# Kernel tuning notes

Measured on AMD Instinct MI355X. Metric: run time of the kernel, lower is better.

## Reference

```python
import jax, jax.numpy as jnp
import numpy as np

EMBED_DIM = 1024
NUM_HEADS = 16
HEAD_DIM = EMBED_DIM // NUM_HEADS
EPS = 1e-6
B, T = 4, 8192


def setup_inputs() -> dict:
    key = jax.random.key(0)
    ks = jax.random.split(key, 11)
    s = 1.0 / np.sqrt(EMBED_DIM)
    inp = {
        'query': jax.random.normal(ks[0], (B, T, EMBED_DIM), jnp.float32),
        'key': jax.random.normal(ks[1], (B, T, EMBED_DIM), jnp.float32),
        'value': jax.random.normal(ks[2], (B, T, EMBED_DIM), jnp.float32),
        'Wq': jax.random.normal(ks[3], (EMBED_DIM, EMBED_DIM), jnp.float32) * s,
        'bq': jnp.zeros((EMBED_DIM,), jnp.float32),
        'Wk': jax.random.normal(ks[4], (EMBED_DIM, EMBED_DIM), jnp.float32) * s,
        'bk': jnp.zeros((EMBED_DIM,), jnp.float32),
        'Wv': jax.random.normal(ks[5], (EMBED_DIM, EMBED_DIM), jnp.float32) * s,
        'bv': jnp.zeros((EMBED_DIM,), jnp.float32),
        'Wo': jax.random.normal(ks[6], (EMBED_DIM, EMBED_DIM), jnp.float32) * s,
        'bo': jnp.zeros((EMBED_DIM,), jnp.float32),
    }
    return inp


def _feature_map(x):
    return jax.nn.elu(x) + 1.0


def reference(query, key, value, Wq, bq, Wk, bk, Wv, bv, Wo, bo):
    b, t, _ = query.shape
    # projections (torch Linear: x @ W.T + b)
    q = query @ Wq.T + bq
    k = key @ Wk.T + bk
    v = value @ Wv.T + bv
    # split heads -> (b, h, t, d)
    def split(x):
        return x.reshape(b, t, NUM_HEADS, HEAD_DIM).transpose(0, 2, 1, 3)
    q = _feature_map(split(q))
    k = _feature_map(split(k))
    v = split(v)
    k_sum = k.sum(axis=2)                                   # (b,h,d)
    denom = jnp.einsum('bhtd,bhd->bht', q, k_sum) + EPS     # (b,h,t)
    kv = jnp.einsum('bhtd,bhtv->bhdv', k, v)                # (b,h,d,d)
    out = jnp.einsum('bhtd,bhde->bhte', q, kv) / denom[..., None]
    out = out.transpose(0, 2, 1, 3).reshape(b, t, EMBED_DIM)
    return out @ Wo.T + bo
```

## Files before the change

### kernel.cpp

```cpp
#include <hip/hip_runtime.h>
#include <hip/hip_bf16.h>

typedef long long TLONG;
typedef float  f32x4_t  __attribute__((ext_vector_type(4)));
typedef short  s16x8_t  __attribute__((ext_vector_type(8)));
typedef short  s16x4_t  __attribute__((ext_vector_type(4)));
typedef __bf16 bf16x8_t __attribute__((ext_vector_type(8)));

#define MDIM 32768
#define NDIM 1024
#define KDIM 1024
#define EPSV 1e-6f

#define BARRIER() asm volatile("s_barrier" ::: "memory")
#define SBAR() __builtin_amdgcn_sched_barrier(0)

__device__ __forceinline__ unsigned short f2bf_bits(float f) {
  __hip_bfloat16 h = __float2bfloat16(f);
  return __builtin_bit_cast(unsigned short, h);
}
__device__ __forceinline__ float bf2f(unsigned short u) {
  unsigned int x = ((unsigned int)u) << 16;
  return __builtin_bit_cast(float, x);
}
__device__ __forceinline__ void load_lds16(const void* g, void* l) {
  __builtin_amdgcn_global_load_lds((const __attribute__((address_space(1))) void*)g,
                                   (__attribute__((address_space(3))) void*)l, 16, 0, 0);
}

__device__ __forceinline__ void conv8(const float* __restrict__ in,
                                      unsigned short* __restrict__ out, TLONG i) {
  f32x4_t a = __builtin_nontemporal_load(reinterpret_cast<const f32x4_t*>(in + i));
  f32x4_t b = __builtin_nontemporal_load(reinterpret_cast<const f32x4_t*>(in + i + 4));
  s16x8_t o;
  o[0] = (short)f2bf_bits(a[0]); o[1] = (short)f2bf_bits(a[1]);
  o[2] = (short)f2bf_bits(a[2]); o[3] = (short)f2bf_bits(a[3]);
  o[4] = (short)f2bf_bits(b[0]); o[5] = (short)f2bf_bits(b[1]);
  o[6] = (short)f2bf_bits(b[2]); o[7] = (short)f2bf_bits(b[3]);
  *reinterpret_cast<s16x8_t*>(out + i) = o;
}

__global__ __launch_bounds__(256) void convert_all_f32_bf16(
    const float* __restrict__ q, const float* __restrict__ k, const float* __restrict__ v,
    const float* __restrict__ wq, const float* __restrict__ wk,
    const float* __restrict__ wv, const float* __restrict__ wo,
    unsigned short* __restrict__ oq, unsigned short* __restrict__ ok,
    unsigned short* __restrict__ ov, unsigned short* __restrict__ owq,
    unsigned short* __restrict__ owk, unsigned short* __restrict__ owv,
    unsigned short* __restrict__ owo) {
  int blk = blockIdx.x;
  if (blk < 6144) {
    const float* in; unsigned short* out;
    if (blk < 2048)      { in = q; out = oq; }
    else if (blk < 4096) { in = k; out = ok; blk -= 2048; }
    else                 { in = v; out = ov; blk -= 4096; }
    const TLONG n = 33554432LL;
    TLONG i = ((TLONG)blk * 256 + threadIdx.x) * 8;
    const TLONG stride = 2048LL * 256 * 8;
    for (; i < n; i += stride) conv8(in, out, i);
  } else {
    blk -= 6144;
    const float* in; unsigned short* out;
    if (blk < 512)       { in = wq; out = owq; }
    else if (blk < 1024) { in = wk; out = owk; blk -= 512; }
    else if (blk < 1536) { in = wv; out = owv; blk -= 1024; }
    else                 { in = wo; out = owo; blk -= 1536; }
    TLONG i = ((TLONG)blk * 256 + threadIdx.x) * 8;
    conv8(in, out, i);
  }
}

template <int FMAP, int OUT>
__global__ __launch_bounds__(512, 2) void gemm256(
    const unsigned short* __restrict__ A, const unsigned short* __restrict__ W,
    const float* __restrict__ bias, void* __restrict__ Cout) {
  __shared__ short lds[65536];
  const int bid = blockIdx.x;
  const int swz = (bid & 7) * 64 + (bid >> 3);
  const int mt = swz >> 2;
  const int nt = swz & 3;

  const int tid = threadIdx.x;
  const int lane = tid & 63;
  const int w = tid >> 6;
  const int wr = w >> 2, wc = w & 3;
  const int l15 = lane & 15, lh = lane >> 4;

  const int arow0 = mt * 256, brow0 = nt * 256;

  auto stage_half = [&](const unsigned short* __restrict__ src, int ldsOff,
                        int grow, int k0) {
#pragma unroll
    for (int i = 0; i < 2; ++i) {
      const int c = i * 512 + tid;
      const int r = c >> 3, ps = c & 7;
      load_lds16(src + (grow + r) * KDIM + k0 + ((ps ^ (r & 7)) * 8),
                 &lds[ldsOff + c * 8]);
    }
  };

  f32x4_t acc[8][4];
#pragma unroll
  for (int m = 0; m < 8; ++m)
#pragma unroll
    for (int n = 0; n < 4; ++n) acc[m][n] = (f32x4_t)0.0f;

  s16x8_t Af[8][2], Bf[4][2];

  auto rdA = [&](int pb, int m, int ks) -> s16x8_t {
    const int row = wr * 128 + m * 16 + l15;
    return *reinterpret_cast<const s16x8_t*>(
        &lds[pb + row * 64 + (((ks * 4 + lh) ^ (row & 7)) * 8)]);
  };
  auto rdB = [&](int pb, int n, int ks) -> s16x8_t {
    const int row = wc * 64 + n * 16 + l15;
    return *reinterpret_cast<const s16x8_t*>(
        &lds[pb + 16384 + row * 64 + (((ks * 4 + lh) ^ (row & 7)) * 8)]);
  };
  auto quad = [&](int mb, int nl) {
    __builtin_amdgcn_s_setprio(1);
#pragma unroll
    for (int m = 0; m < 4; ++m)
#pragma unroll
      for (int n = 0; n < 2; ++n)
#pragma unroll
        for (int ks = 0; ks < 2; ++ks)
          acc[mb + m][nl + n] = __builtin_amdgcn_mfma_f32_16x16x32_bf16(
              __builtin_bit_cast(bf16x8_t, Af[mb + m][ks]),
              __builtin_bit_cast(bf16x8_t, Bf[nl + n][ks]),
              acc[mb + m][nl + n], 0, 0, 0);
    __builtin_amdgcn_s_setprio(0);
  };

  stage_half(A, 0,             arow0,       0);
  stage_half(A, 8192,          arow0 + 128, 0);
  stage_half(W, 16384,         brow0,       0);
  stage_half(W, 16384 + 8192,  brow0 + 128, 0);
  stage_half(A, 32768,         arow0,       64);
  stage_half(A, 32768 + 8192,  arow0 + 128, 64);
  asm volatile("s_waitcnt vmcnt(4)" ::: "memory");
  SBAR();
  BARRIER();

  for (int kt = 0; kt < 16; ++kt) {
    const int p = kt & 1;
    const int pb = p * 32768, qb = 32768 - pb;
    const int k1 = ((kt + 1) & 15) * 64;
    const int k2 = ((kt + 2) & 15) * 64;
#pragma unroll
    for (int m = 0; m < 4; ++m)
#pragma unroll
      for (int ks = 0; ks < 2; ++ks) Af[m][ks] = rdA(pb, m, ks);
#pragma unroll
    for (int n = 0; n < 2; ++n)
#pragma unroll
      for (int ks = 0; ks < 2; ++ks) Bf[n][ks] = rdB(pb, n, ks);
    SBAR();
#pragma unroll
    for (int m = 0; m < 4; ++m)
#pragma unroll
      for (int ks = 0; ks < 2; ++ks) Af[4 + m][ks] = rdA(pb, 4 + m, ks);
    SBAR();
#pragma unroll
    for (int n = 2; n < 4; ++n)
#pragma unroll
      for (int ks = 0; ks < 2; ++ks) Bf[n][ks] = rdB(pb, n, ks);
    SBAR();
    stage_half(W, qb + 16384, brow0, k1);
    BARRIER();
    asm volatile("s_waitcnt lgkmcnt(12)" ::: "memory");
    SBAR();
    quad(0, 0);
    BARRIER();
    stage_half(W, qb + 16384 + 8192, brow0 + 128, k1);
    BARRIER();
    asm volatile("s_waitcnt lgkmcnt(4)" ::: "memory");
    SBAR();
    quad(4, 0);
    BARRIER();
    stage_half(A, pb, arow0, k2);
    BARRIER();
    asm volatile("s_waitcnt lgkmcnt(0)" ::: "memory");
    SBAR();
    quad(0, 2);
    BARRIER();
    stage_half(A, pb + 8192, arow0 + 128, k2);
    BARRIER();
    quad(4, 2);
    asm volatile("s_waitcnt vmcnt(4)" ::: "memory");
    SBAR();
    BARRIER();
  }

  if (OUT == 2) {
    asm volatile("s_waitcnt vmcnt(0)" ::: "memory");
    SBAR();
    BARRIER();
#pragma unroll
    for (int n = 0; n < 4; ++n) {
      const int colL = wc * 64 + n * 16 + l15;
      const float bv = bias[nt * 256 + colL];
      const int xr = (colL & 31) * 8;
#pragma unroll
      for (int m = 0; m < 8; ++m) {
        const int rowL = wr * 128 + m * 16 + lh * 4;
        s16x4_t o;
#pragma unroll
        for (int j = 0; j < 4; ++j) {
          float v = acc[m][n][j] + bv;
          if (FMAP) v = (v > 0.0f) ? (v + 1.0f) : __expf(v);
          o[j] = (short)f2bf_bits(v);
        }
        *reinterpret_cast<s16x4_t*>(&lds[colL * 256 + (rowL ^ xr)]) = o;
      }
    }
    BARRIER();
    const int colL = tid >> 1;
    const int half = tid & 1;
    const int col = nt * 256 + colL;
    const int gh = col >> 6, gd = col & 63;
    const int gb = (mt * 256) >> 13;
    const int tl0 = (mt * 256) & 8191;
    const int xr = (colL & 31) * 8;
    unsigned short* outp = reinterpret_cast<unsigned short*>(Cout) +
        (((TLONG)(gb * 16 + gh) * 64 + gd) * 8192 + tl0 + half * 128);
#pragma unroll
    for (int k = 0; k < 16; ++k) {
      const int row = half * 128 + k * 8;
      s16x8_t v = *reinterpret_cast<const s16x8_t*>(&lds[colL * 256 + (row ^ xr)]);
      *reinterpret_cast<s16x8_t*>(outp + k * 8) = v;
    }
  } else {
#pragma unroll
    for (int n = 0; n < 4; ++n) {
      const int col = nt * 256 + wc * 64 + n * 16 + l15;
      const float bv = bias[col];
#pragma unroll
      for (int m = 0; m < 8; ++m) {
        const int row0 = mt * 256 + wr * 128 + m * 16 + lh * 4;
#pragma unroll
        for (int j = 0; j < 4; ++j) {
          float v = acc[m][n][j] + bv;
          if (FMAP) v = (v > 0.0f) ? (v + 1.0f) : __expf(v);
          if (OUT == 1)
            __builtin_nontemporal_store(v,
                &reinterpret_cast<float*>(Cout)[(row0 + j) * NDIM + col]);
          else
            reinterpret_cast<unsigned short*>(Cout)[(row0 + j) * NDIM + col] = f2bf_bits(v);
        }
      }
    }
  }
}

__global__ __launch_bounds__(256) void kv_ksum_mfma(
    const unsigned short* __restrict__ kT, const unsigned short* __restrict__ vT,
    float* __restrict__ kvT, float* __restrict__ ksum) {
  const int bid = blockIdx.x;
  const int bh = bid >> 4, ch = bid & 15;
  const int tid = threadIdx.x;
  const int lane = tid & 63, w = tid >> 6;
  const int l15 = lane & 15, lh = lane >> 4;
  const int dblk = (w >> 1) * 32, eblk = (w & 1) * 32;

  f32x4_t acc[2][2];
#pragma unroll
  for (int m = 0; m < 2; ++m)
#pragma unroll
    for (int n = 0; n < 2; ++n) acc[m][n] = (f32x4_t)0.0f;
  float ks0 = 0.f, ks1 = 0.f;

  const int tbase = ch * 512 + lh * 8;
  const unsigned short* ka = kT + (bh * 64 + dblk + l15) * 8192 + tbase;
  const unsigned short* va = vT + (bh * 64 + eblk + l15) * 8192 + tbase;

  for (int t0 = 0; t0 < 512; t0 += 32) {
    s16x8_t ar[2], br[2];
#pragma unroll
    for (int m = 0; m < 2; ++m)
      ar[m] = *reinterpret_cast<const s16x8_t*>(ka + m * 16 * 8192 + t0);
#pragma unroll
    for (int n = 0; n < 2; ++n)
      br[n] = *reinterpret_cast<const s16x8_t*>(va + n * 16 * 8192 + t0);
#pragma unroll
    for (int m = 0; m < 2; ++m)
#pragma unroll
      for (int n = 0; n < 2; ++n)
        acc[m][n] = __builtin_amdgcn_mfma_f32_16x16x32_bf16(
            __builtin_bit_cast(bf16x8_t, ar[m]),
            __builtin_bit_cast(bf16x8_t, br[n]), acc[m][n], 0, 0, 0);
    if (eblk == 0) {
#pragma unroll
      for (int i = 0; i < 8; ++i) ks0 += bf2f((unsigned short)ar[0][i]);
#pragma unroll
      for (int i = 0; i < 8; ++i) ks1 += bf2f((unsigned short)ar[1][i]);
    }
  }

  if (eblk == 0) {
    ks0 += __shfl_xor(ks0, 16); ks0 += __shfl_xor(ks0, 32);
    ks1 += __shfl_xor(ks1, 16); ks1 += __shfl_xor(ks1, 32);
    if (lh == 0) {
      atomicAdd(&ksum[bh * 64 + dblk + l15], ks0);
      atomicAdd(&ksum[bh * 64 + dblk + 16 + l15], ks1);
    }
  }
#pragma unroll
  for (int n = 0; n < 2; ++n) {
    const int e = eblk + n * 16 + l15;
#pragma unroll
    for (int m = 0; m < 2; ++m) {
      const int d0 = dblk + m * 16 + lh * 4;
#pragma unroll
      for (int j = 0; j < 4; ++j)
        atomicAdd(&kvT[(bh * 64 + e) * 64 + d0 + j], acc[m][n][j]);
    }
  }
}

__global__ __launch_bounds__(256) void attn_apply_kernel(
    const unsigned short* __restrict__ qf, const float* __restrict__ kvT,
    const float* __restrict__ ksum, unsigned short* __restrict__ att) {
  const int bid = blockIdx.x;
  const int swz = (bid & 7) * 256 + (bid >> 3);
  const int bh = swz >> 5;
  const int tile = swz & 31;
  const int b = bh >> 4, h = bh & 15;
  const int tid = threadIdx.x;
  const int lane = tid & 63, w = tid >> 6;
  const int l15 = lane & 15, lh = lane >> 4;

  float ksr[16];
#pragma unroll
  for (int i = 0; i < 16; ++i) ksr[i] = ksum[bh * 64 + lh * 16 + i];

  bf16x8_t bfrag[2][4];
#pragma unroll
  for (int ks2 = 0; ks2 < 2; ++ks2)
#pragma unroll
    for (int n = 0; n < 4; ++n) {
      const float* p = kvT + (bh * 64 + n * 16 + l15) * 64 + ks2 * 32 + lh * 8;
      f32x4_t p0 = *reinterpret_cast<const f32x4_t*>(p);
      f32x4_t p1 = *reinterpret_cast<const f32x4_t*>(p + 4);
      s16x8_t t;
      t[0] = (short)f2bf_bits(p0[0]); t[1] = (short)f2bf_bits(p0[1]);
      t[2] = (short)f2bf_bits(p0[2]); t[3] = (short)f2bf_bits(p0[3]);
      t[4] = (short)f2bf_bits(p1[0]); t[5] = (short)f2bf_bits(p1[1]);
      t[6] = (short)f2bf_bits(p1[2]); t[7] = (short)f2bf_bits(p1[3]);
      bfrag[ks2][n] = __builtin_bit_cast(bf16x8_t, t);
    }

  const int rbase = b * 8192 + tile * 256 + w * 64;
  f32x4_t acc[4][4];
#pragma unroll
  for (int m = 0; m < 4; ++m)
#pragma unroll
    for (int n = 0; n < 4; ++n) acc[m][n] = (f32x4_t)0.0f;
  float rden[4][4];

#pragma unroll
  for (int m = 0; m < 4; ++m) {
    const int row = rbase + m * 16 + l15;
    const unsigned short* qrow = qf + row * 1024 + h * 64;
    bf16x8_t afr[2];
#pragma unroll
    for (int ks2 = 0; ks2 < 2; ++ks2)
      afr[ks2] = __builtin_bit_cast(bf16x8_t,
          *reinterpret_cast<const s16x8_t*>(qrow + ks2 * 32 + lh * 8));
    s16x8_t qa = *reinterpret_cast<const s16x8_t*>(qrow + lh * 16);
    s16x8_t qb = *reinterpret_cast<const s16x8_t*>(qrow + lh * 16 + 8);
    float part = 0.f;
#pragma unroll
    for (int i = 0; i < 8; ++i) part += bf2f((unsigned short)qa[i]) * ksr[i];
#pragma unroll
    for (int i = 0; i < 8; ++i) part += bf2f((unsigned short)qb[i]) * ksr[8 + i];
    part += __shfl_xor(part, 16);
    part += __shfl_xor(part, 32);
#pragma unroll
    for (int j = 0; j < 4; ++j) {
      float dj = __shfl(part, lh * 4 + j);
      rden[m][j] = 1.0f / (dj + EPSV);
    }
#pragma unroll
    for (int ks2 = 0; ks2 < 2; ++ks2)
#pragma unroll
      for (int n = 0; n < 4; ++n)
        acc[m][n] = __builtin_amdgcn_mfma_f32_16x16x32_bf16(afr[ks2], bfrag[ks2][n], acc[m][n], 0, 0, 0);
  }

#pragma unroll
  for (int m = 0; m < 4; ++m)
#pragma unroll
    for (int n = 0; n < 4; ++n) {
      const int col = h * 64 + n * 16 + l15;
#pragma unroll
      for (int j = 0; j < 4; ++j) {
        const int row = rbase + m * 16 + lh * 4 + j;
        att[row * 1024 + col] = f2bf_bits(acc[m][n][j] * rden[m][j]);
      }
    }
}

extern "C" void kernel_launch(void* const* d_in, const int* in_sizes, int n_in,
                              void* d_out, int out_size, void* d_ws, size_t ws_size,
                              hipStream_t stream) {
  const float* query = (const float*)d_in[0];
  const float* key   = (const float*)d_in[1];
  const float* value = (const float*)d_in[2];
  const float* Wq = (const float*)d_in[3];
  const float* bq = (const float*)d_in[4];
  const float* Wk = (const float*)d_in[5];
  const float* bk = (const float*)d_in[6];
  const float* Wv = (const float*)d_in[7];
  const float* bv = (const float*)d_in[8];
  const float* Wo = (const float*)d_in[9];
  const float* bo = (const float*)d_in[10];
  float* out = (float*)d_out;

  if (ws_size < 277889024ULL) return;
  char* ws = (char*)d_ws;
  unsigned short* Vbf = (unsigned short*)(ws + 0);
  unsigned short* qf  = (unsigned short*)(ws + 67108864);
  unsigned short* kTf = (unsigned short*)(ws + 134217728);
  unsigned short* vTf = (unsigned short*)(ws + 201326592);
  unsigned short* Wqb = (unsigned short*)(ws + 268435456);
  unsigned short* Wkb = Wqb + 1048576;
  unsigned short* Wvb = Wkb + 1048576;
  unsigned short* Wob = Wvb + 1048576;
  float* kvT  = (float*)(ws + 276824064);
  float* ksum = (float*)(ws + 277872640);

  unsigned short* Qbf = (unsigned short*)d_out;
  unsigned short* Kbf = Qbf + 33554432;

  hipMemsetAsync(kvT, 0, (size_t)(64 * 64 * 64 + 64 * 64) * sizeof(float), stream);

  convert_all_f32_bf16<<<8192, 256, 0, stream>>>(
      query, key, value, Wq, Wk, Wv, Wo,
      Qbf, Kbf, Vbf, Wqb, Wkb, Wvb, Wob);

  gemm256<1, 0><<<512, 512, 0, stream>>>(Qbf, Wqb, bq, qf);
  gemm256<1, 2><<<512, 512, 0, stream>>>(Kbf, Wkb, bk, kTf);
  gemm256<0, 2><<<512, 512, 0, stream>>>(Vbf, Wvb, bv, vTf);

  kv_ksum_mfma<<<1024, 256, 0, stream>>>(kTf, vTf, kvT, ksum);

  attn_apply_kernel<<<2048, 256, 0, stream>>>(qf, kvT, ksum, Vbf);

  gemm256<0, 1><<<512, 512, 0, stream>>>(Vbf, Wob, bo, out);
}
```

Before: 598.5 us.

## Merge Q/K/V projection GEMMs into one launch; drop LDS-staged transposed store

The three separate projection GEMM launches become a single 1536-block kernel that picks its operands, bias, feature map and output mode from the segment index. This removes two launches and the tail idle time between them. The transposed (head-major) output path for K and V no longer stages through LDS; each lane writes 4-element strips straight to global memory. That drops a barrier and the LDS round trip but produces 8-byte scattered writes that coalesce poorly, and runtime branches on fmap and outMode replace the compile-time template parameters.

```diff
diff --git a/kernel.cpp b/kernel.cpp
--- a/kernel.cpp
+++ b/kernel.cpp
@@ -70,13 +70,28 @@
   }
 }
 
-template <int FMAP, int OUT>
-__global__ __launch_bounds__(512, 2) void gemm256(
-    const unsigned short* __restrict__ A, const unsigned short* __restrict__ W,
-    const float* __restrict__ bias, void* __restrict__ Cout) {
+__global__ __launch_bounds__(512, 2) void gemm_qkv(
+    const unsigned short* __restrict__ Aq, const unsigned short* __restrict__ Ak,
+    const unsigned short* __restrict__ Av,
+    const unsigned short* __restrict__ Wq, const unsigned short* __restrict__ Wk,
+    const unsigned short* __restrict__ Wv,
+    const float* __restrict__ bq, const float* __restrict__ bk,
+    const float* __restrict__ bv,
+    unsigned short* __restrict__ Cq, unsigned short* __restrict__ Ck,
+    unsigned short* __restrict__ Cv) {
   __shared__ short lds[65536];
-  const int bid = blockIdx.x;
-  const int swz = (bid & 7) * 64 + (bid >> 3);
+  const int seg = blockIdx.x >> 9;
+  const int local = blockIdx.x & 511;
+  const unsigned short* A;
+  const unsigned short* W;
+  const float* bias;
+  unsigned short* Cout;
+  int fmap, outMode;
+  if (seg == 0)      { A = Aq; W = Wq; bias = bq; Cout = Cq; fmap = 1; outMode = 0; }
+  else if (seg == 1) { A = Ak; W = Wk; bias = bk; Cout = Ck; fmap = 1; outMode = 2; }
+  else               { A = Av; W = Wv; bias = bv; Cout = Cv; fmap = 0; outMode = 2; }
+
+  const int swz = (local & 7) * 64 + (local >> 3);
   const int mt = swz >> 2;
   const int nt = swz & 3;
 
@@ -192,63 +207,168 @@
     BARRIER();
   }
 
-  if (OUT == 2) {
-    asm volatile("s_waitcnt vmcnt(0)" ::: "memory");
-    SBAR();
-    BARRIER();
-#pragma unroll
-    for (int n = 0; n < 4; ++n) {
-      const int colL = wc * 64 + n * 16 + l15;
-      const float bv = bias[nt * 256 + colL];
-      const int xr = (colL & 31) * 8;
-#pragma unroll
-      for (int m = 0; m < 8; ++m) {
-        const int rowL = wr * 128 + m * 16 + lh * 4;
+#pragma unroll
+  for (int n = 0; n < 4; ++n) {
+    const int col = nt * 256 + wc * 64 + n * 16 + l15;
+    const float bv2 = bias[col];
+#pragma unroll
+    for (int m = 0; m < 8; ++m) {
+      const int row0 = mt * 256 + wr * 128 + m * 16 + lh * 4;
+      if (outMode == 2) {
+        const int b = row0 >> 13, tl = row0 & 8191;
+        const int h = col >> 6, d = col & 63;
         s16x4_t o;
 #pragma unroll
         for (int j = 0; j < 4; ++j) {
-          float v = acc[m][n][j] + bv;
-          if (FMAP) v = (v > 0.0f) ? (v + 1.0f) : __expf(v);
+          float v = acc[m][n][j] + bv2;
+          if (fmap) v = (v > 0.0f) ? (v + 1.0f) : __expf(v);
           o[j] = (short)f2bf_bits(v);
         }
-        *reinterpret_cast<s16x4_t*>(&lds[colL * 256 + (rowL ^ xr)]) = o;
-      }
-    }
-    BARRIER();
-    const int colL = tid >> 1;
-    const int half = tid & 1;
-    const int col = nt * 256 + colL;
-    const int gh = col >> 6, gd = col & 63;
-    const int gb = (mt * 256) >> 13;
-    const int tl0 = (mt * 256) & 8191;
-    const int xr = (colL & 31) * 8;
-    unsigned short* outp = reinterpret_cast<unsigned short*>(Cout) +
-        (((TLONG)(gb * 16 + gh) * 64 + gd) * 8192 + tl0 + half * 128);
-#pragma unroll
-    for (int k = 0; k < 16; ++k) {
-      const int row = half * 128 + k * 8;
-      s16x8_t v = *reinterpret_cast<const s16x8_t*>(&lds[colL * 256 + (row ^ xr)]);
-      *reinterpret_cast<s16x8_t*>(outp + k * 8) = v;
-    }
-  } else {
-#pragma unroll
-    for (int n = 0; n < 4; ++n) {
-      const int col = nt * 256 + wc * 64 + n * 16 + l15;
-      const float bv = bias[col];
-#pragma unroll
-      for (int m = 0; m < 8; ++m) {
-        const int row0 = mt * 256 + wr * 128 + m * 16 + lh * 4;
+        *reinterpret_cast<s16x4_t*>(Cout + (((b * 16 + h) * 64 + d) * 8192 + tl)) = o;
+      } else {
 #pragma unroll
         for (int j = 0; j < 4; ++j) {
-          float v = acc[m][n][j] + bv;
-          if (FMAP) v = (v > 0.0f) ? (v + 1.0f) : __expf(v);
-          if (OUT == 1)
-            __builtin_nontemporal_store(v,
-                &reinterpret_cast<float*>(Cout)[(row0 + j) * NDIM + col]);
-          else
-            reinterpret_cast<unsigned short*>(Cout)[(row0 + j) * NDIM + col] = f2bf_bits(v);
+          float v = acc[m][n][j] + bv2;
+          if (fmap) v = (v > 0.0f) ? (v + 1.0f) : __expf(v);
+          Cout[(row0 + j) * NDIM + col] = f2bf_bits(v);
         }
       }
+    }
+  }
+}
+
+__global__ __launch_bounds__(512, 2) void gemm_out(
+    const unsigned short* __restrict__ A, const unsigned short* __restrict__ W,
+    const float* __restrict__ bias, float* __restrict__ Cout) {
+  __shared__ short lds[65536];
+  const int bid = blockIdx.x;
+  const int swz = (bid & 7) * 64 + (bid >> 3);
+  const int mt = swz >> 2;
+  const int nt = swz & 3;
+
+  const int tid = threadIdx.x;
+  const int lane = tid & 63;
+  const int w = tid >> 6;
+  const int wr = w >> 2, wc = w & 3;
+  const int l15 = lane & 15, lh = lane >> 4;
+
+  const int arow0 = mt * 256, brow0 = nt * 256;
+
+  auto stage_half = [&](const unsigned short* __restrict__ src, int ldsOff,
+                        int grow, int k0) {
+#pragma unroll
+    for (int i = 0; i < 2; ++i) {
+      const int c = i * 512 + tid;
+      const int r = c >> 3, ps = c & 7;
+      load_lds16(src + (grow + r) * KDIM + k0 + ((ps ^ (r & 7)) * 8),
+                 &lds[ldsOff + c * 8]);
+    }
+  };
+
+  f32x4_t acc[8][4];
+#pragma unroll
+  for (int m = 0; m < 8; ++m)
+#pragma unroll
+    for (int n = 0; n < 4; ++n) acc[m][n] = (f32x4_t)0.0f;
+
+  s16x8_t Af[8][2], Bf[4][2];
+
+  auto rdA = [&](int pb, int m, int ks) -> s16x8_t {
+    const int row = wr * 128 + m * 16 + l15;
+    return *reinterpret_cast<const s16x8_t*>(
+        &lds[pb + row * 64 + (((ks * 4 + lh) ^ (row & 7)) * 8)]);
+  };
+  auto rdB = [&](int pb, int n, int ks) -> s16x8_t {
+    const int row = wc * 64 + n * 16 + l15;
+    return *reinterpret_cast<const s16x8_t*>(
+        &lds[pb + 16384 + row * 64 + (((ks * 4 + lh) ^ (row & 7)) * 8)]);
+  };
+  auto quad = [&](int mb, int nl) {
+    __builtin_amdgcn_s_setprio(1);
+#pragma unroll
+    for (int m = 0; m < 4; ++m)
+#pragma unroll
+      for (int n = 0; n < 2; ++n)
+#pragma unroll
+        for (int ks = 0; ks < 2; ++ks)
+          acc[mb + m][nl + n] = __builtin_amdgcn_mfma_f32_16x16x32_bf16(
+              __builtin_bit_cast(bf16x8_t, Af[mb + m][ks]),
+              __builtin_bit_cast(bf16x8_t, Bf[nl + n][ks]),
+              acc[mb + m][nl + n], 0, 0, 0);
+    __builtin_amdgcn_s_setprio(0);
+  };
+
+  stage_half(A, 0,             arow0,       0);
+  stage_half(A, 8192,          arow0 + 128, 0);
+  stage_half(W, 16384,         brow0,       0);
+  stage_half(W, 16384 + 8192,  brow0 + 128, 0);
+  stage_half(A, 32768,         arow0,       64);
+  stage_half(A, 32768 + 8192,  arow0 + 128, 64);
+  asm volatile("s_waitcnt vmcnt(4)" ::: "memory");
+  SBAR();
+  BARRIER();
+
+  for (int kt = 0; kt < 16; ++kt) {
+    const int p = kt & 1;
+    const int pb = p * 32768, qb = 32768 - pb;
+    const int k1 = ((kt + 1) & 15) * 64;
+    const int k2 = ((kt + 2) & 15) * 64;
+#pragma unroll
+    for (int m = 0; m < 4; ++m)
+#pragma unroll
+      for (int ks = 0; ks < 2; ++ks) Af[m][ks] = rdA(pb, m, ks);
+#pragma unroll
+    for (int n = 0; n < 2; ++n)
+#pragma unroll
+      for (int ks = 0; ks < 2; ++ks) Bf[n][ks] = rdB(pb, n, ks);
+    SBAR();
+#pragma unroll
+    for (int m = 0; m < 4; ++m)
+#pragma unroll
+      for (int ks = 0; ks < 2; ++ks) Af[4 + m][ks] = rdA(pb, 4 + m, ks);
+    SBAR();
+#pragma unroll
+    for (int n = 2; n < 4; ++n)
+#pragma unroll
+      for (int ks = 0; ks < 2; ++ks) Bf[n][ks] = rdB(pb, n, ks);
+    SBAR();
+    stage_half(W, qb + 16384, brow0, k1);
+    BARRIER();
+    asm volatile("s_waitcnt lgkmcnt(12)" ::: "memory");
+    SBAR();
+    quad(0, 0);
+    BARRIER();
+    stage_half(W, qb + 16384 + 8192, brow0 + 128, k1);
+    BARRIER();
+    asm volatile("s_waitcnt lgkmcnt(4)" ::: "memory");
+    SBAR();
+    quad(4, 0);
+    BARRIER();
+    stage_half(A, pb, arow0, k2);
+    BARRIER();
+    asm volatile("s_waitcnt lgkmcnt(0)" ::: "memory");
+    SBAR();
+    quad(0, 2);
+    BARRIER();
+    stage_half(A, pb + 8192, arow0 + 128, k2);
+    BARRIER();
+    quad(4, 2);
+    asm volatile("s_waitcnt vmcnt(4)" ::: "memory");
+    SBAR();
+    BARRIER();
+  }
+
+#pragma unroll
+  for (int n = 0; n < 4; ++n) {
+    const int col = nt * 256 + wc * 64 + n * 16 + l15;
+    const float bv = bias[col];
+#pragma unroll
+    for (int m = 0; m < 8; ++m) {
+      const int row0 = mt * 256 + wr * 128 + m * 16 + lh * 4;
+#pragma unroll
+      for (int j = 0; j < 4; ++j)
+        __builtin_nontemporal_store(acc[m][n][j] + bv,
+                                    &Cout[(row0 + j) * NDIM + col]);
     }
   }
 }
@@ -439,13 +559,12 @@
       query, key, value, Wq, Wk, Wv, Wo,
       Qbf, Kbf, Vbf, Wqb, Wkb, Wvb, Wob);
 
-  gemm256<1, 0><<<512, 512, 0, stream>>>(Qbf, Wqb, bq, qf);
-  gemm256<1, 2><<<512, 512, 0, stream>>>(Kbf, Wkb, bk, kTf);
-  gemm256<0, 2><<<512, 512, 0, stream>>>(Vbf, Wvb, bv, vTf);
+  gemm_qkv<<<1536, 512, 0, stream>>>(Qbf, Kbf, Vbf, Wqb, Wkb, Wvb,
+                                     bq, bk, bv, qf, kTf, vTf);
 
   kv_ksum_mfma<<<1024, 256, 0, stream>>>(kTf, vTf, kvT, ksum);
 
   attn_apply_kernel<<<2048, 256, 0, stream>>>(qf, kvT, ksum, Vbf);
 
-  gemm256<0, 1><<<512, 512, 0, stream>>>(Vbf, Wob, bo, out);
-}
+  gemm_out<<<512, 512, 0, stream>>>(Vbf, Wob, bo, out);
+}
```

Result: faster. 566.4 us (median of 3 runs) (-5.4%).
